# Optimization experiments

Measured on AMD Instinct MI355X. Metric: run time of the kernel, lower is better.

Reference implementation:

```python
import jax, jax.numpy as jnp
import numpy as np

LOG_2PI = 1.8378770664093453

def norm_logpdf(x, mean, std):
    z = (x - mean) / std
    return -0.5 * z * z - jnp.log(std) - 0.5 * LOG_2PI

def setup_inputs() -> dict:
    key = jax.random.key(0)
    ks = jax.random.split(key, 9)
    B, D, H, O = 32768, 512, 20, 5  # batch, in_features, spn in_features, spn out_features
    x = jax.random.normal(ks[0], (B, D), dtype=jnp.float32)
    # fc1: kaiming-normal init as in the original
    W1 = jax.random.normal(ks[1], (H, D), dtype=jnp.float32) * np.float32(np.sqrt(2.0 / D))
    b1 = jnp.zeros((H,), jnp.float32)
    # Per-neuron Gaussian leaf params (two Gaussians per feature per neuron)
    means0 = jax.random.normal(ks[2], (O, H), dtype=jnp.float32)
    means1 = jax.random.normal(ks[3], (O, H), dtype=jnp.float32)
    stds0 = jax.random.uniform(ks[4], (O, H), dtype=jnp.float32, minval=0.1, maxval=1.0)
    stds1 = jax.random.uniform(ks[5], (O, H), dtype=jnp.float32, minval=0.1, maxval=1.0)
    # Sum-node mixture weights: [O, H, H, 2], normalized over last axis, stored in log-space
    w = jax.random.uniform(ks[6], (O, H, H, 2), dtype=jnp.float32, minval=0.01, maxval=1.0)
    log_w = jnp.log(w / w.sum(axis=-1, keepdims=True))
    W2 = jax.random.normal(ks[7], (1, O), dtype=jnp.float32) * np.float32(np.sqrt(2.0 / O))
    b2 = jnp.zeros((1,), jnp.float32)
    return dict(x=x, W1=W1, b1=b1, means0=means0, stds0=stds0,
                means1=means1, stds1=stds1, log_w=log_w, W2=W2, b2=b2)

def reference(x, W1, b1, means0, stds0, means1, stds1, log_w, W2, b2):
    # fc1 + ReLU: [B, 20]
    h = jax.nn.relu(x @ W1.T + b1)
    # Gaussian leaf log-likelihoods per neuron: [B, O, H]
    L0 = norm_logpdf(h[:, None, :], means0[None], stds0[None])
    L1 = norm_logpdf(h[:, None, :], means1[None], stds1[None])
    # Pairwise product nodes (log-space = sums): [B, O, H, H]
    P0 = L0[:, :, :, None] + L0[:, :, None, :]
    P1 = L1[:, :, :, None] + L1[:, :, None, :]
    # Sum nodes: weighted mixture of the two product nodes, in log-space
    S = jnp.logaddexp(log_w[None, ..., 0] + P0, log_w[None, ..., 1] + P1)
    # Root product node: sum over all H*H sum-node children -> [B, O]
    root = S.sum(axis=(2, 3))
    # log(-x), global max - x, fc2, sigmoid
    y = jnp.log(-root)
    y = jnp.max(y) - y
    return jax.nn.sigmoid(y @ W2.T + b2)
```

## Files before the change

kernel.cpp:

```cpp
#include <hip/hip_runtime.h>

#define OFF_CST   16
#define OFF_BASEW 640
#define OFF_LWD   656
#define OFF_W1T   4096
#define OFF_HT    16384
#define OFF_YT    (16384 + 20*32768)
#define NB        32768

__device__ __forceinline__ unsigned enc_f(float f) {
  unsigned u = __float_as_uint(f);
  return (u & 0x80000000u) ? ~u : (u | 0x80000000u);
}
__device__ __forceinline__ float dec_f(unsigned u) {
  return __uint_as_float((u & 0x80000000u) ? (u & 0x7fffffffu) : ~u);
}

__global__ void k0_prep(const float* __restrict__ W1,
                        const float* __restrict__ m0, const float* __restrict__ s0,
                        const float* __restrict__ m1, const float* __restrict__ s1,
                        const float* __restrict__ lw, float* __restrict__ wf) {
  int t = threadIdx.x;
  if (t == 0) ((unsigned*)wf)[0] = 0u;
  for (int idx = t; idx < 10240; idx += 320) {
    int j = idx >> 9, k = idx & 511;
    wf[OFF_W1T + k * 20 + j] = W1[idx];
  }
  if (t < 100) {
    float sd0 = s0[t], sd1 = s1[t];
    float* c = wf + OFF_CST + t * 6;
    c[0] = m0[t]; c[1] = 1.0f / sd0; c[2] = -logf(sd0) - 0.91893853320467267f;
    c[3] = m1[t]; c[4] = 1.0f / sd1; c[5] = -logf(sd1) - 0.91893853320467267f;
  }
  int wv = t >> 6, ln = t & 63;
  float sum = 0.f;
  for (int p = ln; p < 400; p += 64) {
    float w0 = lw[(wv * 400 + p) * 2];
    float w1 = lw[(wv * 400 + p) * 2 + 1];
    wf[OFF_LWD + wv * 400 + p] = w0 - w1;
    sum += w0;
  }
  #pragma unroll
  for (int off = 32; off; off >>= 1) sum += __shfl_xor(sum, off);
  if (ln == 0) wf[OFF_BASEW + wv] = sum;
}

__global__ __launch_bounds__(512, 4) void k1_fc1(
    const float* __restrict__ x, const float* __restrict__ b1,
    const float* __restrict__ wf, float* __restrict__ ht) {
  __shared__ float red[8 * 64 * 21];
  int t = threadIdx.x;
  int r = t & 63;
  int kq = __builtin_amdgcn_readfirstlane(t >> 6);
  size_t row = (size_t)blockIdx.x * 64 + r;
  const float4* xp = (const float4*)(x + row * 512 + kq * 64);
  const float* wt = wf + OFF_W1T + kq * 64 * 20;
  float4 xv[16];
  #pragma unroll
  for (int q = 0; q < 16; ++q) xv[q] = xp[q];
  float acc[20];
  #pragma unroll
  for (int j = 0; j < 20; ++j) acc[j] = 0.f;
  #pragma unroll
  for (int q = 0; q < 16; ++q) {
    const float* wp = wt + q * 80;
    #pragma unroll
    for (int j = 0; j < 20; ++j) acc[j] = fmaf(xv[q].x, wp[j], acc[j]);
    #pragma unroll
    for (int j = 0; j < 20; ++j) acc[j] = fmaf(xv[q].y, wp[20 + j], acc[j]);
    #pragma unroll
    for (int j = 0; j < 20; ++j) acc[j] = fmaf(xv[q].z, wp[40 + j], acc[j]);
    #pragma unroll
    for (int j = 0; j < 20; ++j) acc[j] = fmaf(xv[q].w, wp[60 + j], acc[j]);
  }
  float* rp = red + (kq * 64 + r) * 21;
  #pragma unroll
  for (int j = 0; j < 20; ++j) rp[j] = acc[j];
  __syncthreads();
  for (int idx = t; idx < 1280; idx += 512) {
    int r2 = idx & 63, j = idx >> 6;
    float s = b1[j];
    #pragma unroll
    for (int k = 0; k < 8; ++k) s += red[(k * 64 + r2) * 21 + j];
    ht[j * NB + blockIdx.x * 64 + r2] = fmaxf(s, 0.f);
  }
}

__global__ __launch_bounds__(256) void k2_spn(
    const float* __restrict__ wf, float* __restrict__ yt, unsigned* __restrict__ gm) {
  __shared__ float dl[20][256];
  __shared__ float wmax[4];
  int t = threadIdx.x;
  int o = blockIdx.y;
  size_t b = (size_t)blockIdx.x * 256 + t;
  const float* ht = wf + OFF_HT;
  const float* c = wf + OFF_CST + o * 120;
  float delta[20];
  float sL0 = 0.f;
  #pragma unroll
  for (int j = 0; j < 20; ++j) {
    float hv = ht[j * NB + b];
    float z0 = (hv - c[j * 6 + 0]) * c[j * 6 + 1];
    float L0 = fmaf(z0, -0.5f * z0, c[j * 6 + 2]);
    float z1 = (hv - c[j * 6 + 3]) * c[j * 6 + 4];
    float L1 = fmaf(z1, -0.5f * z1, c[j * 6 + 5]);
    float dj = L0 - L1;
    delta[j] = dj;
    dl[j][t] = dj;
    sL0 += L0;
  }
  float baseA = fmaf(40.f, sL0, wf[OFF_BASEW + o]);
  const float* lwd = wf + OFF_LWD + o * 400;
  float accMin = 0.f, accLn = 0.f;
  #pragma unroll 4
  for (int i = 0; i < 20; ++i) {
    float di = dl[i][t];
    const float* lwp = lwd + i * 20;
    float p0 = 1.f, p1 = 1.f, mn0 = 0.f, mn1 = 0.f;
    #pragma unroll
    for (int j = 0; j < 20; ++j) {
      float d = (lwp[j] + di) + delta[j];
      float mnd = fminf(d, 0.f);
      float e = __expf(-fabsf(d));
      float u = 1.f + e;
      if (j & 1) { mn1 += mnd; p1 *= u; } else { mn0 += mnd; p0 *= u; }
    }
    accMin += mn0 + mn1;
    accLn += __logf(p0 * p1);
  }
  float root = baseA - accMin + accLn;
  float y = __logf(-root);
  yt[o * NB + b] = y;
  float m = y;
  #pragma unroll
  for (int off = 32; off; off >>= 1) m = fmaxf(m, __shfl_xor(m, off));
  if ((t & 63) == 0) wmax[t >> 6] = m;
  __syncthreads();
  if (t == 0) {
    float mm = fmaxf(fmaxf(wmax[0], wmax[1]), fmaxf(wmax[2], wmax[3]));
    atomicMax(gm, enc_f(mm));
  }
}

__global__ __launch_bounds__(256) void k3_out(
    const float* __restrict__ wf, const unsigned* __restrict__ gm,
    const float* __restrict__ W2, const float* __restrict__ b2,
    float* __restrict__ out) {
  size_t b = (size_t)blockIdx.x * 256 + threadIdx.x;
  float g = dec_f(*gm);
  const float* yt = wf + OFF_YT;
  float acc = b2[0];
  #pragma unroll
  for (int o = 0; o < 5; ++o)
    acc += (g - yt[o * NB + b]) * W2[o];
  out[b] = 1.0f / (1.0f + __expf(-acc));
}

extern "C" void kernel_launch(void* const* d_in, const int* in_sizes, int n_in,
                              void* d_out, int out_size, void* d_ws, size_t ws_size,
                              hipStream_t stream) {
  const float* x  = (const float*)d_in[0];
  const float* W1 = (const float*)d_in[1];
  const float* b1 = (const float*)d_in[2];
  const float* m0 = (const float*)d_in[3];
  const float* s0 = (const float*)d_in[4];
  const float* m1 = (const float*)d_in[5];
  const float* s1 = (const float*)d_in[6];
  const float* lw = (const float*)d_in[7];
  const float* W2 = (const float*)d_in[8];
  const float* b2 = (const float*)d_in[9];
  float* wf = (float*)d_ws;
  float* out = (float*)d_out;

  k0_prep<<<1, 320, 0, stream>>>(W1, m0, s0, m1, s1, lw, wf);
  k1_fc1<<<512, 512, 0, stream>>>(x, b1, wf, wf + OFF_HT);
  k2_spn<<<dim3(128, 5), 256, 0, stream>>>(wf, wf + OFF_YT, (unsigned*)d_ws);
  k3_out<<<NB / 256, 256, 0, stream>>>(wf, (const unsigned*)d_ws, W2, b2, out);
}
```

Measured before the change: 152.0 us.

## Use base-2 exp/log with min-via-abs identity and parallelize prep kernel

The pairwise logaddexp inner loop now works in base-2 units: log-weight differences and leaf deltas are pre-scaled by log2(e), so exp2 and log2 are used directly. The per-element fminf(d,0) is replaced by accumulating |d|, with the sum of d recovered in closed form from precomputed row sums (min(d,0) = (d-|d|)/2). The prep kernel is spread over 46 blocks instead of one, so the W1 transpose and weight reductions run in parallel. The change adds a little floating-point reordering that could slightly alter rounding.

```diff
diff --git a/kernel.cpp b/kernel.cpp
--- a/kernel.cpp
+++ b/kernel.cpp
@@ -2,11 +2,14 @@
 
 #define OFF_CST   16
 #define OFF_BASEW 640
+#define OFF_SUMD  648
 #define OFF_LWD   656
 #define OFF_W1T   4096
 #define OFF_HT    16384
 #define OFF_YT    (16384 + 20*32768)
 #define NB        32768
+#define LOG2E     1.4426950408889634f
+#define LN2       0.6931471805599453f
 
 __device__ __forceinline__ unsigned enc_f(float f) {
   unsigned u = __float_as_uint(f);
@@ -16,33 +19,50 @@
   return __uint_as_float((u & 0x80000000u) ? (u & 0x7fffffffu) : ~u);
 }
 
-__global__ void k0_prep(const float* __restrict__ W1,
-                        const float* __restrict__ m0, const float* __restrict__ s0,
-                        const float* __restrict__ m1, const float* __restrict__ s1,
-                        const float* __restrict__ lw, float* __restrict__ wf) {
-  int t = threadIdx.x;
-  if (t == 0) ((unsigned*)wf)[0] = 0u;
-  for (int idx = t; idx < 10240; idx += 320) {
+__global__ __launch_bounds__(256) void k0_prep(
+    const float* __restrict__ W1,
+    const float* __restrict__ m0, const float* __restrict__ s0,
+    const float* __restrict__ m1, const float* __restrict__ s1,
+    const float* __restrict__ lw, float* __restrict__ wf) {
+  int t = threadIdx.x, blk = blockIdx.x;
+  if (blk < 40) {
+    int idx = blk * 256 + t;
     int j = idx >> 9, k = idx & 511;
     wf[OFF_W1T + k * 20 + j] = W1[idx];
-  }
+    return;
+  }
+  if (blk < 45) {
+    int o = blk - 40;
+    __shared__ float r0[4], r1[4];
+    float s0w = 0.f, sdw = 0.f;
+    for (int p = t; p < 400; p += 256) {
+      float w0 = lw[(o * 400 + p) * 2];
+      float w1 = lw[(o * 400 + p) * 2 + 1];
+      wf[OFF_LWD + o * 400 + p] = (w0 - w1) * LOG2E;
+      s0w += w0;
+      sdw += w0 - w1;
+    }
+    #pragma unroll
+    for (int off = 32; off; off >>= 1) {
+      s0w += __shfl_xor(s0w, off);
+      sdw += __shfl_xor(sdw, off);
+    }
+    int wv = t >> 6;
+    if ((t & 63) == 0) { r0[wv] = s0w; r1[wv] = sdw; }
+    __syncthreads();
+    if (t == 0) {
+      wf[OFF_BASEW + o] = r0[0] + r0[1] + r0[2] + r0[3];
+      wf[OFF_SUMD  + o] = r1[0] + r1[1] + r1[2] + r1[3];
+    }
+    return;
+  }
+  if (t == 0) ((unsigned*)wf)[0] = 0u;
   if (t < 100) {
     float sd0 = s0[t], sd1 = s1[t];
     float* c = wf + OFF_CST + t * 6;
     c[0] = m0[t]; c[1] = 1.0f / sd0; c[2] = -logf(sd0) - 0.91893853320467267f;
     c[3] = m1[t]; c[4] = 1.0f / sd1; c[5] = -logf(sd1) - 0.91893853320467267f;
   }
-  int wv = t >> 6, ln = t & 63;
-  float sum = 0.f;
-  for (int p = ln; p < 400; p += 64) {
-    float w0 = lw[(wv * 400 + p) * 2];
-    float w1 = lw[(wv * 400 + p) * 2 + 1];
-    wf[OFF_LWD + wv * 400 + p] = w0 - w1;
-    sum += w0;
-  }
-  #pragma unroll
-  for (int off = 32; off; off >>= 1) sum += __shfl_xor(sum, off);
-  if (ln == 0) wf[OFF_BASEW + wv] = sum;
 }
 
 __global__ __launch_bounds__(512, 4) void k1_fc1(
@@ -95,8 +115,8 @@
   size_t b = (size_t)blockIdx.x * 256 + t;
   const float* ht = wf + OFF_HT;
   const float* c = wf + OFF_CST + o * 120;
-  float delta[20];
-  float sL0 = 0.f;
+  float d2[20];
+  float sL0 = 0.f, sd2 = 0.f;
   #pragma unroll
   for (int j = 0; j < 20; ++j) {
     float hv = ht[j * NB + b];
@@ -104,31 +124,33 @@
     float L0 = fmaf(z0, -0.5f * z0, c[j * 6 + 2]);
     float z1 = (hv - c[j * 6 + 3]) * c[j * 6 + 4];
     float L1 = fmaf(z1, -0.5f * z1, c[j * 6 + 5]);
-    float dj = L0 - L1;
-    delta[j] = dj;
-    dl[j][t] = dj;
+    float dj2 = (L0 - L1) * LOG2E;
+    d2[j] = dj2;
+    dl[j][t] = dj2;
     sL0 += L0;
+    sd2 += dj2;
   }
   float baseA = fmaf(40.f, sL0, wf[OFF_BASEW + o]);
-  const float* lwd = wf + OFF_LWD + o * 400;
-  float accMin = 0.f, accLn = 0.f;
+  const float* lwd2 = wf + OFF_LWD + o * 400;
+  float aAbs0 = 0.f, aAbs1 = 0.f, accL2 = 0.f;
   #pragma unroll 4
   for (int i = 0; i < 20; ++i) {
     float di = dl[i][t];
-    const float* lwp = lwd + i * 20;
-    float p0 = 1.f, p1 = 1.f, mn0 = 0.f, mn1 = 0.f;
+    const float* lwp = lwd2 + i * 20;
+    float p0 = 1.f, p1 = 1.f;
     #pragma unroll
     for (int j = 0; j < 20; ++j) {
-      float d = (lwp[j] + di) + delta[j];
-      float mnd = fminf(d, 0.f);
-      float e = __expf(-fabsf(d));
+      float d = (lwp[j] + di) + d2[j];
+      float e = exp2f(-fabsf(d));
       float u = 1.f + e;
-      if (j & 1) { mn1 += mnd; p1 *= u; } else { mn0 += mnd; p0 *= u; }
-    }
-    accMin += mn0 + mn1;
-    accLn += __logf(p0 * p1);
-  }
-  float root = baseA - accMin + accLn;
+      if (j & 1) { aAbs1 += fabsf(d); p1 *= u; }
+      else       { aAbs0 += fabsf(d); p0 *= u; }
+    }
+    accL2 += __log2f(p0 * p1);
+  }
+  float accAbs2 = aAbs0 + aAbs1;
+  float lwdSum = wf[OFF_SUMD + o];
+  float root = baseA - 0.5f * (lwdSum + LN2 * (40.f * sd2 - accAbs2)) + LN2 * accL2;
   float y = __logf(-root);
   yt[o * NB + b] = y;
   float m = y;
@@ -172,7 +194,7 @@
   float* wf = (float*)d_ws;
   float* out = (float*)d_out;
 
-  k0_prep<<<1, 320, 0, stream>>>(W1, m0, s0, m1, s1, lw, wf);
+  k0_prep<<<46, 256, 0, stream>>>(W1, m0, s0, m1, s1, lw, wf);
   k1_fc1<<<512, 512, 0, stream>>>(x, b1, wf, wf + OFF_HT);
   k2_spn<<<dim3(128, 5), 256, 0, stream>>>(wf, wf + OFF_YT, (unsigned*)d_ws);
   k3_out<<<NB / 256, 256, 0, stream>>>(wf, (const unsigned*)d_ws, W2, b2, out);
```

Result: no change. 149.8 us (-1.5%).
